# Kernel tuning notes

Measured on AMD Instinct MI355X. Metric: run time of the kernel, lower is better.

## Reference

```python
import jax, jax.numpy as jnp
import numpy as np

HIDDEN = 2048
N_HEADS = 16
HEAD_DIM = 128
N_KV_HEADS = 4
MAX_POS = 4096
NEG_INF = -1e9


def _fixed_pos_embedding(features, length):
    # matches generate_fixed_pos_embedding: freqs over arange(0, features, 2)/features
    fraction = jnp.arange(0, features, 2, dtype=jnp.float32) / features
    timescale = 10000.0 ** fraction
    inv_freq = 1.0 / timescale
    sinusoid = jnp.einsum('i,j->ij', jnp.arange(length, dtype=jnp.float32), inv_freq)
    sinusoid = jnp.concatenate([sinusoid, sinusoid], axis=-1)  # [length, features]
    return jnp.sin(sinusoid), jnp.cos(sinusoid)


def setup_inputs() -> dict:
    key = jax.random.key(0)
    k0, k1, k2, k3, k4 = jax.random.split(key, 5)
    B, S = 2, 2048
    hidden_states = jax.random.normal(k0, (B, S, HIDDEN), dtype=jnp.float32)
    # causal additive mask [B,1,S,S]; module forces mask[:, :, :, 0] = 0
    causal = jnp.where(jnp.tril(jnp.ones((S, S), dtype=bool)), 0.0, NEG_INF).astype(jnp.float32)
    causal = causal.at[:, 0].set(0.0)
    attention_mask = jnp.broadcast_to(causal[None, None], (B, 1, S, S))
    std = 0.02
    q_w = jax.random.normal(k1, (N_HEADS * HEAD_DIM, HIDDEN), dtype=jnp.float32) * std
    k_w = jax.random.normal(k2, (N_KV_HEADS * HEAD_DIM, HIDDEN), dtype=jnp.float32) * std
    v_w = jax.random.normal(k3, (N_KV_HEADS * HEAD_DIM, HIDDEN), dtype=jnp.float32) * std
    o_w = jax.random.normal(k4, (HIDDEN, N_HEADS * HEAD_DIM), dtype=jnp.float32) * std
    sin, cos = _fixed_pos_embedding(HEAD_DIM, MAX_POS)
    return {"hidden_states": hidden_states, "attention_mask": attention_mask,
            "q_w": q_w, "k_w": k_w, "v_w": v_w, "o_w": o_w, "sin": sin, "cos": cos}


def _rotate_half(x):
    d = x.shape[-1] // 2
    return jnp.concatenate([-x[..., d:], x[..., :d]], axis=-1)


def reference(hidden_states, attention_mask, q_w, k_w, v_w, o_w, sin, cos):
    B, S, _ = hidden_states.shape
    D = cos.shape[-1]
    H = q_w.shape[0] // D
    KV = k_w.shape[0] // D
    n_rep = H // KV

    # QKV projections (nn.Linear: y = x @ W^T), split into heads: [B,S,h,D]
    q = jnp.einsum('bsh,oh->bso', hidden_states, q_w).reshape(B, S, H, D)
    k = jnp.einsum('bsh,oh->bso', hidden_states, k_w).reshape(B, S, KV, D)
    v = jnp.einsum('bsh,oh->bso', hidden_states, v_w).reshape(B, S, KV, D)

    # rotary embedding (non-decode path: q and k share cos/sin[:S])
    c = cos[:S][None, :, None, :]
    s = sin[:S][None, :, None, :]
    q = q * c + _rotate_half(q) * s
    k = k * c + _rotate_half(k) * s

    # repeat_kv (repeat_interleave along head dim) for GQA
    k = jnp.repeat(k, n_rep, axis=2)  # [B,S,H,D]
    v = jnp.repeat(v, n_rep, axis=2)

    # NOTE: no 1/sqrt(D) scaling -- module uses softmax_scale=1.0
    scores = jnp.einsum('bqhd,bkhd->bhqk', q, k) + attention_mask
    weights = jax.nn.softmax(scores.astype(jnp.float32), axis=-1).astype(q.dtype)
    attn = jnp.einsum('bhqk,bkhd->bqhd', weights, v).reshape(B, S, H * D)
    return jnp.einsum('bso,ho->bsh', attn, o_w)
```

## Files before the change

### kernel.cpp

```cpp
#include <hip/hip_runtime.h>

typedef __bf16 bf16x8 __attribute__((ext_vector_type(8)));
typedef float f32x4 __attribute__((ext_vector_type(4)));

#define LOG2E 1.44269504088896340736f

#define GLDS16(g, l) __builtin_amdgcn_global_load_lds(                         \
    (const __attribute__((address_space(1))) unsigned int*)(g),                \
    (__attribute__((address_space(3))) unsigned int*)(l), 16, 0, 0)

__global__ __launch_bounds__(256) void split_matrix(
    const float* __restrict__ src, __bf16* __restrict__ dh, __bf16* __restrict__ dl)
{
    const size_t t = (size_t)(blockIdx.x * 256 + threadIdx.x) * 8;
    float4 a = *(const float4*)(src + t);
    float4 b = *(const float4*)(src + t + 4);
    float f[8] = {a.x, a.y, a.z, a.w, b.x, b.y, b.z, b.w};
    bf16x8 h, l;
#pragma unroll
    for (int i = 0; i < 8; ++i) {
        __bf16 hh = (__bf16)f[i];
        h[i] = hh; l[i] = (__bf16)(f[i] - (float)hh);
    }
    *(bf16x8*)(dh + t) = h;
    *(bf16x8*)(dl + t) = l;
}

__global__ __launch_bounds__(256) void gemm_planes(
    const __bf16* __restrict__ Ah, const __bf16* __restrict__ Al,
    const __bf16* __restrict__ Bh, const __bf16* __restrict__ Bl,
    float* __restrict__ C, int K, int ldc)
{
    __shared__ __bf16 sAh[128 * 32], sAl[128 * 32];
    __shared__ __bf16 sBh[128 * 32], sBl[128 * 32];

    const int tid  = threadIdx.x;
    const int lane = tid & 63;
    const int wave = tid >> 6;
    const int m0 = blockIdx.y * 128;
    const int n0 = blockIdx.x * 128;

    const int sr  = wave * 32 + (lane >> 2);
    const int sc  = (lane & 3) * 8;
    const __bf16* ga0 = Ah + (size_t)(m0 + sr) * K + sc;
    const __bf16* ga1 = ga0 + (size_t)16 * K;
    const __bf16* gA0 = Al + (size_t)(m0 + sr) * K + sc;
    const __bf16* gA1 = gA0 + (size_t)16 * K;
    const __bf16* gb0 = Bh + (size_t)(n0 + sr) * K + sc;
    const __bf16* gb1 = gb0 + (size_t)16 * K;
    const __bf16* gB0 = Bl + (size_t)(n0 + sr) * K + sc;
    const __bf16* gB1 = gB0 + (size_t)16 * K;
    __bf16* la0 = &sAh[(wave * 32) * 32];
    __bf16* la1 = &sAh[(wave * 32 + 16) * 32];
    __bf16* lA0 = &sAl[(wave * 32) * 32];
    __bf16* lA1 = &sAl[(wave * 32 + 16) * 32];
    __bf16* lb0 = &sBh[(wave * 32) * 32];
    __bf16* lb1 = &sBh[(wave * 32 + 16) * 32];
    __bf16* lB0 = &sBl[(wave * 32) * 32];
    __bf16* lB1 = &sBl[(wave * 32 + 16) * 32];

    f32x4 acc[4][4];
    for (int mi = 0; mi < 4; ++mi)
        for (int ni = 0; ni < 4; ++ni)
            acc[mi][ni] = (f32x4){0.f, 0.f, 0.f, 0.f};

    const int wm = (wave & 1) * 64;
    const int wn = (wave >> 1) * 64;
    const int fr = lane & 15;
    const int fc = (lane >> 4) * 8;
    const int dr = (lane >> 4) * 4;

    for (int k0 = 0; k0 < K; k0 += 32) {
        GLDS16(ga0, la0); GLDS16(ga1, la1);
        GLDS16(gA0, lA0); GLDS16(gA1, lA1);
        GLDS16(gb0, lb0); GLDS16(gb1, lb1);
        GLDS16(gB0, lB0); GLDS16(gB1, lB1);
        ga0 += 32; ga1 += 32; gA0 += 32; gA1 += 32;
        gb0 += 32; gb1 += 32; gB0 += 32; gB1 += 32;
        __syncthreads();

        bf16x8 afh[4], afl[4], bfh[4], bfl[4];
#pragma unroll
        for (int i = 0; i < 4; ++i) {
            afh[i] = *(const bf16x8*)&sAh[(wm + i * 16 + fr) * 32 + fc];
            afl[i] = *(const bf16x8*)&sAl[(wm + i * 16 + fr) * 32 + fc];
            bfh[i] = *(const bf16x8*)&sBh[(wn + i * 16 + fr) * 32 + fc];
            bfl[i] = *(const bf16x8*)&sBl[(wn + i * 16 + fr) * 32 + fc];
        }
#pragma unroll
        for (int mi = 0; mi < 4; ++mi)
#pragma unroll
            for (int ni = 0; ni < 4; ++ni) {
                acc[mi][ni] = __builtin_amdgcn_mfma_f32_16x16x32_bf16(
                    afh[mi], bfh[ni], acc[mi][ni], 0, 0, 0);
                acc[mi][ni] = __builtin_amdgcn_mfma_f32_16x16x32_bf16(
                    afl[mi], bfh[ni], acc[mi][ni], 0, 0, 0);
                acc[mi][ni] = __builtin_amdgcn_mfma_f32_16x16x32_bf16(
                    afh[mi], bfl[ni], acc[mi][ni], 0, 0, 0);
            }
        __syncthreads();
    }

    for (int mi = 0; mi < 4; ++mi)
        for (int ni = 0; ni < 4; ++ni)
            for (int r = 0; r < 4; ++r) {
                int row = m0 + wm + mi * 16 + dr + r;
                int col = n0 + wn + ni * 16 + fr;
                C[(size_t)row * ldc + col] = acc[mi][ni][r];
            }
}

__global__ __launch_bounds__(256) void rope_q(
    float* __restrict__ qkv,
    const float* __restrict__ sinp, const float* __restrict__ cosp)
{
    int t = blockIdx.x * 256 + threadIdx.x;
    int row = t >> 10;
    int rem = t & 1023;
    int col = (rem >> 6) * 128 + (rem & 63);
    int s = row & 2047;
    int d = col & 127;

    float* p = qkv + (size_t)row * 3072 + col;
    float x0  = p[0];
    float x1  = p[64];
    float c0  = cosp[s * 128 + d];
    float c1  = cosp[s * 128 + d + 64];
    float sn0 = sinp[s * 128 + d];
    float sn1 = sinp[s * 128 + d + 64];
    p[0]  = x0 * c0 - x1 * sn0;
    p[64] = x1 * c1 + x0 * sn1;
}

__global__ __launch_bounds__(256) void prep_kv(
    const float* __restrict__ qkv,
    const float* __restrict__ sinp, const float* __restrict__ cosp,
    __bf16* __restrict__ ksp, __bf16* __restrict__ vtsp)
{
    __shared__ float vs[32][132];

    const int tid = threadIdx.x;
    const int kb  = blockIdx.x;
    const int kvh = blockIdx.y;
    const int b   = blockIdx.z;

    {
        const int key = tid >> 1;
        const int dh  = (tid & 1) * 32;
        const int pos = kb * 128 + key;
        const int ksw = key & 7;
        const float* src = qkv + (size_t)(b * 2048 + pos) * 3072 + 2048 + kvh * 128;
        __bf16* dst = ksp + ((size_t)((b * 4 + kvh) * 2048) + pos) * 256;
        const float* cp = cosp + pos * 128;
        const float* sp = sinp + pos * 128;
#pragma unroll
        for (int g = 0; g < 4; ++g) {
            int d0 = dh + g * 8;
            float4 x0a = *(const float4*)(src + d0);
            float4 x0b = *(const float4*)(src + d0 + 4);
            float4 x1a = *(const float4*)(src + d0 + 64);
            float4 x1b = *(const float4*)(src + d0 + 68);
            float4 c0a = *(const float4*)(cp + d0);
            float4 c0b = *(const float4*)(cp + d0 + 4);
            float4 c1a = *(const float4*)(cp + d0 + 64);
            float4 c1b = *(const float4*)(cp + d0 + 68);
            float4 s0a = *(const float4*)(sp + d0);
            float4 s0b = *(const float4*)(sp + d0 + 4);
            float4 s1a = *(const float4*)(sp + d0 + 64);
            float4 s1b = *(const float4*)(sp + d0 + 68);
            float x0[8] = {x0a.x,x0a.y,x0a.z,x0a.w,x0b.x,x0b.y,x0b.z,x0b.w};
            float x1[8] = {x1a.x,x1a.y,x1a.z,x1a.w,x1b.x,x1b.y,x1b.z,x1b.w};
            float c0[8] = {c0a.x,c0a.y,c0a.z,c0a.w,c0b.x,c0b.y,c0b.z,c0b.w};
            float c1[8] = {c1a.x,c1a.y,c1a.z,c1a.w,c1b.x,c1b.y,c1b.z,c1b.w};
            float s0[8] = {s0a.x,s0a.y,s0a.z,s0a.w,s0b.x,s0b.y,s0b.z,s0b.w};
            float s1[8] = {s1a.x,s1a.y,s1a.z,s1a.w,s1b.x,s1b.y,s1b.z,s1b.w};
            bf16x8 h0, l0, h1, l1;
#pragma unroll
            for (int i = 0; i < 8; ++i) {
                float y0 = x0[i] * c0[i] - x1[i] * s0[i];
                float y1 = x1[i] * c1[i] + x0[i] * s1[i];
                __bf16 hh0 = (__bf16)y0;
                __bf16 hh1 = (__bf16)y1;
                h0[i] = hh0; l0[i] = (__bf16)(y0 - (float)hh0);
                h1[i] = hh1; l1[i] = (__bf16)(y1 - (float)hh1);
            }
            const int bb = d0 >> 3;
            *(bf16x8*)(dst + ((bb        ^ ksw) << 3)) = h0;
            *(bf16x8*)(dst + (((bb + 8)  ^ ksw) << 3)) = h1;
            *(bf16x8*)(dst + (((bb + 16) ^ ksw) << 3)) = l0;
            *(bf16x8*)(dst + (((bb + 24) ^ ksw) << 3)) = l1;
        }
    }

    for (int st = 0; st < 4; ++st) {
        __syncthreads();
        {
            const int key = tid >> 3;
            const int dc  = (tid & 7) * 16;
            const float* vsrc = qkv + (size_t)(b * 2048 + kb * 128 + st * 32 + key) * 3072
                                + 2560 + kvh * 128 + dc;
            float4 v0 = *(const float4*)(vsrc);
            float4 v1 = *(const float4*)(vsrc + 4);
            float4 v2 = *(const float4*)(vsrc + 8);
            float4 v3 = *(const float4*)(vsrc + 12);
            *(float4*)&vs[key][dc]      = v0;
            *(float4*)&vs[key][dc + 4]  = v1;
            *(float4*)&vs[key][dc + 8]  = v2;
            *(float4*)&vs[key][dc + 12] = v3;
        }
        __syncthreads();
        {
            const int plane = tid >> 7;
            const int d     = tid & 127;
            bf16x8 ob[4];
#pragma unroll
            for (int k = 0; k < 32; ++k) {
                float x = vs[k][d];
                __bf16 hh = (__bf16)x;
                ob[k >> 3][k & 7] = plane ? (__bf16)(x - (float)hh) : hh;
            }
            const int rV  = plane * 128 + d;
            const int vsw = (d >> 1) & 3;
            __bf16* dst = vtsp + ((size_t)((b * 4 + kvh) * 64 + kb * 4 + st)) * 8192
                               + (size_t)rV * 32;
            *(bf16x8*)(dst + ((0 ^ vsw) << 3)) = ob[0];
            *(bf16x8*)(dst + ((1 ^ vsw) << 3)) = ob[1];
            *(bf16x8*)(dst + ((2 ^ vsw) << 3)) = ob[2];
            *(bf16x8*)(dst + ((3 ^ vsw) << 3)) = ob[3];
        }
    }
}

__global__ __launch_bounds__(256, 3) void flash_attn(
    const float* __restrict__ qkv,
    const __bf16* __restrict__ ksp,
    const __bf16* __restrict__ vtsp,
    __bf16* __restrict__ attnh, __bf16* __restrict__ attnl)
{
    __shared__ __bf16 Ks[32 * 256];
    __shared__ __bf16 Vt[256 * 32];
    __shared__ float  Psf[4][2][16][36];

    const int tid  = threadIdx.x;
    const int lane = tid & 63;
    const int wave = tid >> 6;
    const int id   = blockIdx.x;
    const int pair = id & 7;
    const int kvh  = pair & 3;
    const int b    = pair >> 2;
    const int u    = id >> 3;
    const int qb   = (u >> 5) ? (u & 31) : 63 - (u & 31);
    const int h    = kvh * 4 + wave;

    const int fr  = lane & 15;
    const int g   = lane >> 4;
    const int fc  = g * 8;
    const int dr  = g * 4;
    const int frs = fr & 7;

    bf16x8 aqh[2][4], aql[2][4];
    for (int rs = 0; rs < 2; ++rs) {
        const size_t qrow = (size_t)(b * 2048 + qb * 32 + rs * 16 + fr) * 3072 + h * 128;
        for (int ks = 0; ks < 4; ++ks) {
            float4 qv[2];
            qv[0] = *(const float4*)(qkv + qrow + ks * 32 + fc);
            qv[1] = *(const float4*)(qkv + qrow + ks * 32 + fc + 4);
            const float* qf = (const float*)qv;
            bf16x8 h8, l8;
#pragma unroll
            for (int i = 0; i < 8; ++i) {
                float x = qf[i];
                __bf16 hh = (__bf16)x;
                h8[i] = hh; l8[i] = (__bf16)(x - (float)hh);
            }
            aqh[rs][ks] = h8; aql[rs][ks] = l8;
        }
    }

    bf16x8 ones;
#pragma unroll
    for (int i = 0; i < 8; ++i) ones[i] = (__bf16)1.0f;

    f32x4 o[2][8];
    for (int rs = 0; rs < 2; ++rs)
        for (int dg = 0; dg < 8; ++dg) o[rs][dg] = (f32x4){0.f, 0.f, 0.f, 0.f};
    f32x4 ls[2] = {(f32x4){0.f,0.f,0.f,0.f}, (f32x4){0.f,0.f,0.f,0.f}};

    const int ntiles = qb + 1;
    const __bf16* kbase = ksp + (size_t)(b * 4 + kvh) * 2048 * 256;
    const __bf16* vbase = vtsp + (size_t)(b * 4 + kvh) * 64 * 8192;

    for (int kt = 0; kt < ntiles; ++kt) {
        const int k0 = kt * 32;

        __syncthreads();
        {
            const __bf16* kg = kbase + (size_t)k0 * 256 + wave * 2048 + lane * 8;
            const __bf16* vg = vbase + (size_t)kt * 8192 + wave * 2048 + lane * 8;
            __bf16* kl = &Ks[wave * 2048];
            __bf16* vl = &Vt[wave * 2048];
            GLDS16(kg,        kl);
            GLDS16(kg + 512,  kl + 512);
            GLDS16(kg + 1024, kl + 1024);
            GLDS16(kg + 1536, kl + 1536);
            GLDS16(vg,        vl);
            GLDS16(vg + 512,  vl + 512);
            GLDS16(vg + 1024, vl + 1024);
            GLDS16(vg + 1536, vl + 1536);
        }
        __syncthreads();

        f32x4 s[2][2];
        s[0][0] = s[0][1] = s[1][0] = s[1][1] = (f32x4){0.f, 0.f, 0.f, 0.f};
        __builtin_amdgcn_s_setprio(1);
#pragma unroll
        for (int ks = 0; ks < 4; ++ks) {
            const int bh = ks * 4 + g;
            bf16x8 b0h = *(const bf16x8*)&Ks[fr * 256        + ((bh        ^ frs) << 3)];
            bf16x8 b0l = *(const bf16x8*)&Ks[fr * 256        + (((bh + 16) ^ frs) << 3)];
            bf16x8 b1h = *(const bf16x8*)&Ks[(16 + fr) * 256 + ((bh        ^ frs) << 3)];
            bf16x8 b1l = *(const bf16x8*)&Ks[(16 + fr) * 256 + (((bh + 16) ^ frs) << 3)];
#pragma unroll
            for (int rs = 0; rs < 2; ++rs) {
                s[rs][0] = __builtin_amdgcn_mfma_f32_16x16x32_bf16(aqh[rs][ks], b0h, s[rs][0], 0, 0, 0);
                s[rs][0] = __builtin_amdgcn_mfma_f32_16x16x32_bf16(aql[rs][ks], b0h, s[rs][0], 0, 0, 0);
                s[rs][0] = __builtin_amdgcn_mfma_f32_16x16x32_bf16(aqh[rs][ks], b0l, s[rs][0], 0, 0, 0);
                s[rs][1] = __builtin_amdgcn_mfma_f32_16x16x32_bf16(aqh[rs][ks], b1h, s[rs][1], 0, 0, 0);
                s[rs][1] = __builtin_amdgcn_mfma_f32_16x16x32_bf16(aql[rs][ks], b1h, s[rs][1], 0, 0, 0);
                s[rs][1] = __builtin_amdgcn_mfma_f32_16x16x32_bf16(aqh[rs][ks], b1l, s[rs][1], 0, 0, 0);
            }
        }
        __builtin_amdgcn_s_setprio(0);

        const bool diag = (kt == ntiles - 1);
#pragma unroll
        for (int rs = 0; rs < 2; ++rs) {
            f32x4 s0 = s[rs][0], s1 = s[rs][1];
            if (diag) {
#pragma unroll
                for (int r = 0; r < 4; ++r) {
                    const int qg = qb * 32 + rs * 16 + dr + r;
                    if (k0 + fr > qg)      s0[r] = -1e30f;
                    if (k0 + 16 + fr > qg) s1[r] = -1e30f;
                }
            }
#pragma unroll
            for (int r = 0; r < 4; ++r) {
                s0[r] = exp2f(s0[r] * LOG2E);
                s1[r] = exp2f(s1[r] * LOG2E);
            }
#pragma unroll
            for (int r = 0; r < 4; ++r) {
                Psf[wave][rs][dr + r][fr]      = s0[r];
                Psf[wave][rs][dr + r][16 + fr] = s1[r];
            }
        }
        asm volatile("s_waitcnt lgkmcnt(0)" ::: "memory");
        float4 pva[2], pvb[2];
        pva[0] = *(const float4*)&Psf[wave][0][fr][fc];
        pva[1] = *(const float4*)&Psf[wave][0][fr][fc + 4];
        pvb[0] = *(const float4*)&Psf[wave][1][fr][fc];
        pvb[1] = *(const float4*)&Psf[wave][1][fr][fc + 4];
        asm volatile("s_waitcnt lgkmcnt(0)" ::: "memory");
        bf16x8 ph[2], pl[2];
        {
            const float* pf0 = (const float*)pva;
            const float* pf1 = (const float*)pvb;
#pragma unroll
            for (int i = 0; i < 8; ++i) {
                float x0 = pf0[i], x1 = pf1[i];
                __bf16 h0 = (__bf16)x0, h1 = (__bf16)x1;
                ph[0][i] = h0; pl[0][i] = (__bf16)(x0 - (float)h0);
                ph[1][i] = h1; pl[1][i] = (__bf16)(x1 - (float)h1);
            }
        }

        __builtin_amdgcn_s_setprio(1);
        ls[0] = __builtin_amdgcn_mfma_f32_16x16x32_bf16(ph[0], ones, ls[0], 0, 0, 0);
        ls[0] = __builtin_amdgcn_mfma_f32_16x16x32_bf16(pl[0], ones, ls[0], 0, 0, 0);
        ls[1] = __builtin_amdgcn_mfma_f32_16x16x32_bf16(ph[1], ones, ls[1], 0, 0, 0);
        ls[1] = __builtin_amdgcn_mfma_f32_16x16x32_bf16(pl[1], ones, ls[1], 0, 0, 0);
#pragma unroll
        for (int dg = 0; dg < 8; ++dg) {
            const int d0 = dg * 16 + fr;
            const int sw = (g ^ ((d0 >> 1) & 3)) << 3;
            bf16x8 bvh = *(const bf16x8*)&Vt[d0 * 32 + sw];
            bf16x8 bvl = *(const bf16x8*)&Vt[(d0 + 128) * 32 + sw];
#pragma unroll
            for (int rs = 0; rs < 2; ++rs) {
                o[rs][dg] = __builtin_amdgcn_mfma_f32_16x16x32_bf16(ph[rs], bvh, o[rs][dg], 0, 0, 0);
                o[rs][dg] = __builtin_amdgcn_mfma_f32_16x16x32_bf16(pl[rs], bvh, o[rs][dg], 0, 0, 0);
                o[rs][dg] = __builtin_amdgcn_mfma_f32_16x16x32_bf16(ph[rs], bvl, o[rs][dg], 0, 0, 0);
            }
        }
        __builtin_amdgcn_s_setprio(0);
    }

    for (int rs = 0; rs < 2; ++rs) {
        const size_t orow = (size_t)(b * 2048 + qb * 32 + rs * 16);
        for (int dg = 0; dg < 8; ++dg)
            for (int r = 0; r < 4; ++r) {
                float val = o[rs][dg][r] / ls[rs][r];
                size_t idx = (orow + dr + r) * 2048 + h * 128 + dg * 16 + fr;
                __bf16 hh = (__bf16)val;
                attnh[idx] = hh;
                attnl[idx] = (__bf16)(val - (float)hh);
            }
    }
}

extern "C" void kernel_launch(void* const* d_in, const int* in_sizes, int n_in,
                              void* d_out, int out_size, void* d_ws, size_t ws_size,
                              hipStream_t stream)
{
    const float* hs   = (const float*)d_in[0];
    const float* qw   = (const float*)d_in[2];
    const float* kw   = (const float*)d_in[3];
    const float* vw   = (const float*)d_in[4];
    const float* ow   = (const float*)d_in[5];
    const float* sinp = (const float*)d_in[6];
    const float* cosp = (const float*)d_in[7];
    float* outp = (float*)d_out;

    char* w = (char*)d_ws;
    float*  qkv  = (float*)w;   w += (size_t)4096 * 3072 * 4;
    __bf16* ksp  = (__bf16*)w;  w += (size_t)8 * 2048 * 256 * 2;
    __bf16* vtsp = (__bf16*)w;  w += (size_t)8 * 64 * 8192 * 2;
    __bf16* wqh  = (__bf16*)w;  w += (size_t)3072 * 2048 * 2;
    __bf16* wql  = (__bf16*)w;  w += (size_t)3072 * 2048 * 2;
    __bf16* owh  = (__bf16*)w;  w += (size_t)2048 * 2048 * 2;
    __bf16* owl  = (__bf16*)w;  w += (size_t)2048 * 2048 * 2;
    __bf16* hsh  = (__bf16*)w;  w += (size_t)4096 * 2048 * 2;
    __bf16* hsl  = (__bf16*)w;  w += (size_t)4096 * 2048 * 2;
    __bf16* attnh = hsh;
    __bf16* attnl = hsl;

    split_matrix<<<4096, 256, 0, stream>>>(hs, hsh, hsl);
    split_matrix<<<2048, 256, 0, stream>>>(qw, wqh, wql);
    split_matrix<<<512,  256, 0, stream>>>(kw, wqh + (size_t)2048 * 2048,
                                               wql + (size_t)2048 * 2048);
    split_matrix<<<512,  256, 0, stream>>>(vw, wqh + (size_t)2560 * 2048,
                                               wql + (size_t)2560 * 2048);
    split_matrix<<<2048, 256, 0, stream>>>(ow, owh, owl);

    gemm_planes<<<dim3(24, 32), 256, 0, stream>>>(hsh, hsl, wqh, wql, qkv, 2048, 3072);
    rope_q<<<16384, 256, 0, stream>>>(qkv, sinp, cosp);
    prep_kv<<<dim3(16, 4, 2), 256, 0, stream>>>(qkv, sinp, cosp, ksp, vtsp);
    flash_attn<<<512, 256, 0, stream>>>(qkv, ksp, vtsp, attnh, attnl);
    gemm_planes<<<dim3(16, 32), 256, 0, stream>>>(attnh, attnl, owh, owl, outp, 2048, 2048);
}
```

Baseline: 611.7 us.

## Double-buffer K/V tiles in flash attention and pack P hi/lo split before LDS

Adds two LDS buffers for the K and V tiles, so the global-to-LDS load of the next tile is issued before computing on the current one, with explicit vmcnt waits and barriers. This overlaps memory latency with the MFMA work. The softmax probabilities are now split into bf16 hi/lo pairs before the LDS exchange, packed as 32-bit words with a swizzled layout, which removes the float round trip and the per-lane conversion after the read. Occupancy drops from 3 to 2 blocks per CU because of the larger LDS footprint and the lower launch bound.

Result: no change. 600.5 us (-1.8%).

```diff
diff --git a/kernel.cpp b/kernel.cpp
--- a/kernel.cpp
+++ b/kernel.cpp
@@ -231,15 +231,15 @@
     }
 }
 
-__global__ __launch_bounds__(256, 3) void flash_attn(
+__global__ __launch_bounds__(256, 2) void flash_attn(
     const float* __restrict__ qkv,
     const __bf16* __restrict__ ksp,
     const __bf16* __restrict__ vtsp,
     __bf16* __restrict__ attnh, __bf16* __restrict__ attnl)
 {
-    __shared__ __bf16 Ks[32 * 256];
-    __shared__ __bf16 Vt[256 * 32];
-    __shared__ float  Psf[4][2][16][36];
+    __shared__ __bf16 Ks[2][32 * 256];
+    __shared__ __bf16 Vt[2][256 * 32];
+    __shared__ unsigned int Psf[4][2][512];
 
     const int tid  = threadIdx.x;
     const int lane = tid & 63;
@@ -276,6 +276,8 @@
             aqh[rs][ks] = h8; aql[rs][ks] = l8;
         }
     }
+    asm volatile("s_waitcnt vmcnt(0)" ::: "memory");
+    __builtin_amdgcn_sched_barrier(0);
 
     bf16x8 ones;
 #pragma unroll
@@ -287,28 +289,38 @@
     f32x4 ls[2] = {(f32x4){0.f,0.f,0.f,0.f}, (f32x4){0.f,0.f,0.f,0.f}};
 
     const int ntiles = qb + 1;
-    const __bf16* kbase = ksp + (size_t)(b * 4 + kvh) * 2048 * 256;
-    const __bf16* vbase = vtsp + (size_t)(b * 4 + kvh) * 64 * 8192;
+    const __bf16* kg0 = ksp + (size_t)(b * 4 + kvh) * 2048 * 256 + wave * 2048 + lane * 8;
+    const __bf16* vg0 = vtsp + (size_t)(b * 4 + kvh) * 64 * 8192 + wave * 2048 + lane * 8;
+
+    {
+        __bf16* kl = &Ks[0][wave * 2048];
+        __bf16* vl = &Vt[0][wave * 2048];
+        GLDS16(kg0,        kl);       GLDS16(kg0 + 512,  kl + 512);
+        GLDS16(kg0 + 1024, kl + 1024);GLDS16(kg0 + 1536, kl + 1536);
+        GLDS16(vg0,        vl);       GLDS16(vg0 + 512,  vl + 512);
+        GLDS16(vg0 + 1024, vl + 1024);GLDS16(vg0 + 1536, vl + 1536);
+    }
 
     for (int kt = 0; kt < ntiles; ++kt) {
+        if (kt + 1 < ntiles) {
+            const __bf16* kg = kg0 + (size_t)(kt + 1) * 8192;
+            const __bf16* vg = vg0 + (size_t)(kt + 1) * 8192;
+            __bf16* kl = &Ks[(kt + 1) & 1][wave * 2048];
+            __bf16* vl = &Vt[(kt + 1) & 1][wave * 2048];
+            GLDS16(kg,        kl);       GLDS16(kg + 512,  kl + 512);
+            GLDS16(kg + 1024, kl + 1024);GLDS16(kg + 1536, kl + 1536);
+            GLDS16(vg,        vl);       GLDS16(vg + 512,  vl + 512);
+            GLDS16(vg + 1024, vl + 1024);GLDS16(vg + 1536, vl + 1536);
+            asm volatile("s_waitcnt vmcnt(8)" ::: "memory");
+        } else {
+            asm volatile("s_waitcnt vmcnt(0)" ::: "memory");
+        }
+        __builtin_amdgcn_sched_barrier(0);
+        __builtin_amdgcn_s_barrier();
+        __builtin_amdgcn_sched_barrier(0);
+
+        const int buf = kt & 1;
         const int k0 = kt * 32;
-
-        __syncthreads();
-        {
-            const __bf16* kg = kbase + (size_t)k0 * 256 + wave * 2048 + lane * 8;
-            const __bf16* vg = vbase + (size_t)kt * 8192 + wave * 2048 + lane * 8;
-            __bf16* kl = &Ks[wave * 2048];
-            __bf16* vl = &Vt[wave * 2048];
-            GLDS16(kg,        kl);
-            GLDS16(kg + 512,  kl + 512);
-            GLDS16(kg + 1024, kl + 1024);
-            GLDS16(kg + 1536, kl + 1536);
-            GLDS16(vg,        vl);
-            GLDS16(vg + 512,  vl + 512);
-            GLDS16(vg + 1024, vl + 1024);
-            GLDS16(vg + 1536, vl + 1536);
-        }
-        __syncthreads();
 
         f32x4 s[2][2];
         s[0][0] = s[0][1] = s[1][0] = s[1][1] = (f32x4){0.f, 0.f, 0.f, 0.f};
@@ -316,10 +328,10 @@
 #pragma unroll
         for (int ks = 0; ks < 4; ++ks) {
             const int bh = ks * 4 + g;
-            bf16x8 b0h = *(const bf16x8*)&Ks[fr * 256        + ((bh        ^ frs) << 3)];
-            bf16x8 b0l = *(const bf16x8*)&Ks[fr * 256        + (((bh + 16) ^ frs) << 3)];
-            bf16x8 b1h = *(const bf16x8*)&Ks[(16 + fr) * 256 + ((bh        ^ frs) << 3)];
-            bf16x8 b1l = *(const bf16x8*)&Ks[(16 + fr) * 256 + (((bh + 16) ^ frs) << 3)];
+            bf16x8 b0h = *(const bf16x8*)&Ks[buf][fr * 256        + ((bh        ^ frs) << 3)];
+            bf16x8 b0l = *(const bf16x8*)&Ks[buf][fr * 256        + (((bh + 16) ^ frs) << 3)];
+            bf16x8 b1h = *(const bf16x8*)&Ks[buf][(16 + fr) * 256 + ((bh        ^ frs) << 3)];
+            bf16x8 b1l = *(const bf16x8*)&Ks[buf][(16 + fr) * 256 + (((bh + 16) ^ frs) << 3)];
 #pragma unroll
             for (int rs = 0; rs < 2; ++rs) {
                 s[rs][0] = __builtin_amdgcn_mfma_f32_16x16x32_bf16(aqh[rs][ks], b0h, s[rs][0], 0, 0, 0);
@@ -344,34 +356,38 @@
                     if (k0 + 16 + fr > qg) s1[r] = -1e30f;
                 }
             }
+            uint4 w0, w1;
 #pragma unroll
             for (int r = 0; r < 4; ++r) {
-                s0[r] = exp2f(s0[r] * LOG2E);
-                s1[r] = exp2f(s1[r] * LOG2E);
-            }
-#pragma unroll
-            for (int r = 0; r < 4; ++r) {
-                Psf[wave][rs][dr + r][fr]      = s0[r];
-                Psf[wave][rs][dr + r][16 + fr] = s1[r];
-            }
+                float x0 = exp2f(s0[r] * LOG2E);
+                float x1 = exp2f(s1[r] * LOG2E);
+                __bf16 h0 = (__bf16)x0;
+                __bf16 h1 = (__bf16)x1;
+                unsigned u0 = ((unsigned)__builtin_bit_cast(unsigned short, h0) << 16)
+                            |  (unsigned)__builtin_bit_cast(unsigned short, (__bf16)(x0 - (float)h0));
+                unsigned u1 = ((unsigned)__builtin_bit_cast(unsigned short, h1) << 16)
+                            |  (unsigned)__builtin_bit_cast(unsigned short, (__bf16)(x1 - (float)h1));
+                ((unsigned*)&w0)[r] = u0;
+                ((unsigned*)&w1)[r] = u1;
+            }
+            unsigned int* pw = &Psf[wave][rs][0];
+            const int sb = (fr * 4 + g) ^ (((fr >> 3) & 1) << 2);
+            *(uint4*)(pw + sb * 4)        = w0;
+            *(uint4*)(pw + (sb + 64) * 4) = w1;
         }
         asm volatile("s_waitcnt lgkmcnt(0)" ::: "memory");
-        float4 pva[2], pvb[2];
-        pva[0] = *(const float4*)&Psf[wave][0][fr][fc];
-        pva[1] = *(const float4*)&Psf[wave][0][fr][fc + 4];
-        pvb[0] = *(const float4*)&Psf[wave][1][fr][fc];
-        pvb[1] = *(const float4*)&Psf[wave][1][fr][fc + 4];
-        asm volatile("s_waitcnt lgkmcnt(0)" ::: "memory");
+        __builtin_amdgcn_sched_barrier(0);
+
         bf16x8 ph[2], pl[2];
-        {
-            const float* pf0 = (const float*)pva;
-            const float* pf1 = (const float*)pvb;
-#pragma unroll
-            for (int i = 0; i < 8; ++i) {
-                float x0 = pf0[i], x1 = pf1[i];
-                __bf16 h0 = (__bf16)x0, h1 = (__bf16)x1;
-                ph[0][i] = h0; pl[0][i] = (__bf16)(x0 - (float)h0);
-                ph[1][i] = h1; pl[1][i] = (__bf16)(x1 - (float)h1);
+#pragma unroll
+        for (int rs = 0; rs < 2; ++rs) {
+#pragma unroll
+            for (int j = 0; j < 8; ++j) {
+                const int col = fc + j;
+                const int sR  = (col * 4 + (fr >> 2)) ^ ((g & 1) << 2);
+                const unsigned v = Psf[wave][rs][sR * 4 + (fr & 3)];
+                ph[rs][j] = __builtin_bit_cast(__bf16, (unsigned short)(v >> 16));
+                pl[rs][j] = __builtin_bit_cast(__bf16, (unsigned short)(v & 0xffffu));
             }
         }
 
@@ -384,8 +400,8 @@
         for (int dg = 0; dg < 8; ++dg) {
             const int d0 = dg * 16 + fr;
             const int sw = (g ^ ((d0 >> 1) & 3)) << 3;
-            bf16x8 bvh = *(const bf16x8*)&Vt[d0 * 32 + sw];
-            bf16x8 bvl = *(const bf16x8*)&Vt[(d0 + 128) * 32 + sw];
+            bf16x8 bvh = *(const bf16x8*)&Vt[buf][d0 * 32 + sw];
+            bf16x8 bvl = *(const bf16x8*)&Vt[buf][(d0 + 128) * 32 + sw];
 #pragma unroll
             for (int rs = 0; rs < 2; ++rs) {
                 o[rs][dg] = __builtin_amdgcn_mfma_f32_16x16x32_bf16(ph[rs], bvh, o[rs][dg], 0, 0, 0);
@@ -394,6 +410,8 @@
             }
         }
         __builtin_amdgcn_s_setprio(0);
+
+        __builtin_amdgcn_s_barrier();
     }
 
     for (int rs = 0; rs < 2; ++rs) {
```
